# Optimization experiments

Measured on AMD Instinct MI355X. Metric: run time of the kernel, lower is better.

Reference implementation:

```python
import jax, jax.numpy as jnp
import numpy as np

E, TOPK, H, I = 8, 2, 2048, 5632
T = 4096


def setup_inputs() -> dict:
    key = jax.random.key(0)
    k1, k2, k3, k4 = jax.random.split(key, 4)
    hidden_states = jax.random.normal(k1, (T, H), dtype=jnp.float32)
    gate_w = jax.random.normal(k2, (E, H), dtype=jnp.float32) * (1.0 / np.sqrt(H))
    # fused gate+up projection: [E, 2*I, H]
    w13 = jax.random.normal(k3, (E, 2 * I, H), dtype=jnp.float32) * (1.0 / np.sqrt(H))
    # down projection: [E, H, I]
    w2 = jax.random.normal(k4, (E, H, I), dtype=jnp.float32) * (1.0 / np.sqrt(I))
    return {"hidden_states": hidden_states, "gate_w": gate_w, "w13": w13, "w2": w2, "top_k": TOPK}


def reference(hidden_states, gate_w, w13, w2, top_k):
    num_experts = gate_w.shape[0]
    inter = w2.shape[2]
    # router: fp32 gate logits -> softmax -> top-k -> renormalize (FusedMoE renormalize=True)
    logits = hidden_states.astype(jnp.float32) @ gate_w.T          # [T, E]
    probs = jax.nn.softmax(logits, axis=-1)
    vals, idx = jax.lax.top_k(probs, top_k)                        # [T, k]
    vals = vals / jnp.sum(vals, axis=-1, keepdims=True)
    # dense routing weight matrix [T, E] (zero outside top-k)
    dense_w = jnp.sum(jax.nn.one_hot(idx, num_experts, dtype=vals.dtype) * vals[..., None], axis=1)

    def body(acc, inputs):
        w13_e, w2_e, we = inputs                                   # [2I,H], [H,I], [T]
        gu = hidden_states @ w13_e.T                               # [T, 2I]
        g, u = gu[:, :inter], gu[:, inter:]
        h = jax.nn.silu(g) * u                                     # SwiGLU
        y = h @ w2_e.T                                             # [T, H]
        return acc + we[:, None] * y, None

    acc0 = jnp.zeros_like(hidden_states)
    out, _ = jax.lax.scan(body, acc0, (w13, w2, dense_w.T))
    return out
```

## Files before the change

### kernel.cpp

```cpp
#include <hip/hip_runtime.h>

#define T_TOK 4096
#define H_DIM 2048
#define I_DIM 5632
#define NE 8

typedef _Float16 f16;
typedef _Float16 f16x8 __attribute__((ext_vector_type(8)));
typedef float f32x4 __attribute__((ext_vector_type(4)));

#define OFF_META   0
#define OFF_BTOK   256
#define OFF_BW     (256 + 32768)
#define OFF_RE     (256 + 2 * 32768)
#define OFF_RW     (256 + 3 * 32768)
#define OFF_HSB    (256 + 4 * 32768)
#define OFF_WF     (OFF_HSB + (size_t)T_TOK * H_DIM * 2)

typedef const __attribute__((address_space(1))) unsigned int guint;
typedef __attribute__((address_space(3))) unsigned int luint;

__device__ __forceinline__ int swzk(int r, int bir) {
    return (bir & 15) | ((((bir >> 4) ^ r) & 7) << 4);
}

__global__ void cvt_w_kernel(const float* __restrict__ src, f16* __restrict__ dst, int n8) {
    int stride = gridDim.x * blockDim.x;
    for (int i = blockIdx.x * blockDim.x + threadIdx.x; i < n8; i += stride) {
        size_t b = (size_t)i * 8;
        float4 a = *(const float4*)(src + b);
        float4 c = *(const float4*)(src + b + 4);
        f16x8 v;
        v[0] = (f16)a.x; v[1] = (f16)a.y; v[2] = (f16)a.z; v[3] = (f16)a.w;
        v[4] = (f16)c.x; v[5] = (f16)c.y; v[6] = (f16)c.z; v[7] = (f16)c.w;
        *(f16x8*)(dst + b) = v;
    }
}

__global__ void cvt_hs_kernel(const float* __restrict__ hs, f16* __restrict__ hsb) {
    size_t i = ((size_t)blockIdx.x * 256 + threadIdx.x) * 8;
    float4 a = *(const float4*)(hs + i);
    float4 b = *(const float4*)(hs + i + 4);
    f16x8 v;
    v[0] = (f16)a.x; v[1] = (f16)a.y; v[2] = (f16)a.z; v[3] = (f16)a.w;
    v[4] = (f16)b.x; v[5] = (f16)b.y; v[6] = (f16)b.z; v[7] = (f16)b.w;
    *(f16x8*)(hsb + i) = v;
}

__global__ void gate_kernel(const float* __restrict__ hs, const float* __restrict__ gw,
                            int* __restrict__ re, float* __restrict__ rw,
                            int* __restrict__ counts) {
    int lane = threadIdx.x & 63;
    int t = blockIdx.x * 4 + (threadIdx.x >> 6);
    float acc[NE];
#pragma unroll
    for (int e = 0; e < NE; ++e) acc[e] = 0.f;
    const float* x = hs + (size_t)t * H_DIM;
    for (int i = lane; i < H_DIM; i += 64) {
        float xv = x[i];
#pragma unroll
        for (int e = 0; e < NE; ++e) acc[e] += xv * gw[e * H_DIM + i];
    }
#pragma unroll
    for (int e = 0; e < NE; ++e)
        for (int off = 32; off > 0; off >>= 1) acc[e] += __shfl_xor(acc[e], off);
    if (lane == 0) {
        int i1 = 0; float l1 = acc[0];
#pragma unroll
        for (int e = 1; e < NE; ++e) if (acc[e] > l1) { l1 = acc[e]; i1 = e; }
        int i2 = -1; float l2 = -1e30f;
#pragma unroll
        for (int e = 0; e < NE; ++e) if (e != i1 && acc[e] > l2) { l2 = acc[e]; i2 = e; }
        float aa = __expf(l2 - l1);
        float s = 1.f / (1.f + aa);
        re[t * 2] = i1; re[t * 2 + 1] = i2;
        rw[t * 2] = s;  rw[t * 2 + 1] = aa * s;
        atomicAdd(&counts[i1], 1);
        atomicAdd(&counts[i2], 1);
    }
}

__global__ void scan_kernel(int* __restrict__ meta) {
    if (threadIdx.x == 0) {
        int s = 0;
        for (int e = 0; e < NE; ++e) { meta[8 + e] = s; meta[16 + e] = s; s += meta[e]; }
    }
}

__global__ void place_kernel(const int* __restrict__ re, const float* __restrict__ rw,
                             int* __restrict__ cursor, int* __restrict__ btok,
                             float* __restrict__ bwv) {
    int t = blockIdx.x * 256 + threadIdx.x;
    if (t >= T_TOK) return;
#pragma unroll
    for (int s = 0; s < 2; ++s) {
        int e = re[t * 2 + s];
        int p = atomicAdd(&cursor[e], 1);
        btok[p] = t;
        bwv[p] = rw[t * 2 + s];
    }
}

__device__ __forceinline__ void decode_panel(int id, int npx, int e_arg,
                                             int& e, int& bx, int& by) {
    if (e_arg >= 0) { e = e_arg; bx = id >> 5; by = id & 31; return; }
    int sg  = id >> 8;
    int rem = id & 255;
    by = rem >> 3;
    int P = sg * 8 + (rem & 7);
    e = P / npx; bx = P % npx;
}

__global__ __launch_bounds__(256, 2) void gemm1_kernel(
    const f16* __restrict__ w13f, const f16* __restrict__ hsb, f16* __restrict__ hb,
    const int* __restrict__ counts, const int* __restrict__ offs,
    const int* __restrict__ btok, int e_arg, int global_h)
{
    int e, bx, by;
    decode_panel(blockIdx.x, 88, e_arg, e, bx, by);
    const int n_e = counts[e];
    if (by * 128 >= n_e) return;
    const int boff = offs[e];
    const f16* We = (e_arg >= 0) ? w13f : (w13f + (size_t)e * (2 * I_DIM) * H_DIM);

    const int tid = threadIdx.x;
    const int lane = tid & 63;
    const int wid = tid >> 6;
    const int wm = wid >> 1, wn = wid & 1;
    const int l15 = lane & 15;

    __shared__ f16 As0[128 * 64], As1[128 * 64];
    __shared__ f16 Bs0[128 * 64], Bs1[128 * 64];

    const f16* gA[4]; const f16* gB[4]; int dstc[4];
#pragma unroll
    for (int i = 0; i < 4; ++i) {
        int c = i * 256 + tid;
        int r = c >> 3;
        dstc[i] = c * 16;
        int slot = ((c & 7) ^ (r & 7)) * 8;
        int idx = by * 128 + r;
        idx = idx < n_e ? idx : n_e - 1;
        gA[i] = hsb + (size_t)btok[boff + idx] * H_DIM + slot;
        int wrow = (r < 64) ? (bx * 64 + r) : (I_DIM + bx * 64 + (r - 64));
        gB[i] = We + (size_t)wrow * H_DIM + slot;
    }

    f32x4 ag[4][2], au[4][2];
#pragma unroll
    for (int m = 0; m < 4; ++m)
#pragma unroll
        for (int n = 0; n < 2; ++n) { ag[m][n] = (f32x4)0.f; au[m][n] = (f32x4)0.f; }

    const int NT = H_DIM / 64;

#pragma unroll
    for (int i = 0; i < 4; ++i) {
        __builtin_amdgcn_global_load_lds((guint*)gA[i], (luint*)((char*)As0 + dstc[i]), 16, 0, 0);
        __builtin_amdgcn_global_load_lds((guint*)gB[i], (luint*)((char*)Bs0 + dstc[i]), 16, 0, 0);
    }

#define G1T(AR, BR, AW, BW, t)                                                      \
    {                                                                               \
        __syncthreads();    \
        if ((t) + 1 < NT) {                                                         \
            const int k0 = ((t) + 1) * 64;                                          \
            _Pragma("unroll")                                                       \
            for (int i = 0; i < 4; ++i) {                                           \
                __builtin_amdgcn_global_load_lds((guint*)(gA[i] + k0),              \
                    (luint*)((char*)AW + dstc[i]), 16, 0, 0);                       \
                __builtin_amdgcn_global_load_lds((guint*)(gB[i] + k0),              \
                    (luint*)((char*)BW + dstc[i]), 16, 0, 0);                       \
            }                                                                       \
        }                                                                           \
        _Pragma("unroll")                                                           \
        for (int kh = 0; kh < 2; ++kh) {                                            \
            const int kb = kh * 64 + (lane >> 4) * 16;                              \
            f16x8 a[4], bg[2], bu[2];                                               \
            _Pragma("unroll")                                                       \
            for (int m = 0; m < 4; ++m) {                                           \
                int r = wm * 64 + m * 16 + l15;                                     \
                a[m] = *(const f16x8*)((const char*)AR + r * 128 + swzk(r, kb));    \
            }                                                                       \
            _Pragma("unroll")                                                       \
            for (int n = 0; n < 2; ++n) {                                           \
                int rg = wn * 32 + n * 16 + l15;                                    \
                bg[n] = *(const f16x8*)((const char*)BR + rg * 128 + swzk(rg, kb)); \
                int ru = 64 + rg;                                                   \
                bu[n] = *(const f16x8*)((const char*)BR + ru * 128 + swzk(ru, kb)); \
            }                                                                       \
            _Pragma("unroll")                                                       \
            for (int m = 0; m < 4; ++m)                                             \
                _Pragma("unroll")                                                   \
                for (int n = 0; n < 2; ++n) {                                       \
                    ag[m][n] = __builtin_amdgcn_mfma_f32_16x16x32_f16(a[m], bg[n], ag[m][n], 0, 0, 0); \
                    au[m][n] = __builtin_amdgcn_mfma_f32_16x16x32_f16(a[m], bu[n], au[m][n], 0, 0, 0); \
                }                                                                   \
        }                                                                           \
    }

#pragma unroll 1
    for (int kt = 0; kt < NT; kt += 2) {
        G1T(As0, Bs0, As1, Bs1, kt);
        G1T(As1, Bs1, As0, Bs0, kt + 1);
    }
#undef G1T

    const int hbase = (global_h ? boff : 0) + by * 128;
#pragma unroll
    for (int m = 0; m < 4; ++m) {
        int rl0 = wm * 64 + m * 16 + ((lane >> 4) << 2);
#pragma unroll
        for (int r = 0; r < 4; ++r) {
            int rl = rl0 + r;
            if (by * 128 + rl < n_e) {
#pragma unroll
                for (int n = 0; n < 2; ++n) {
                    float g = ag[m][n][r];
                    float u = au[m][n][r];
                    float h = g / (1.f + __expf(-g)) * u;
                    hb[(size_t)(hbase + rl) * I_DIM + bx * 64 + wn * 32 + n * 16 + l15] = (f16)h;
                }
            }
        }
    }
}

__global__ __launch_bounds__(256, 2) void gemm2_kernel(
    const f16* __restrict__ w2f, const f16* __restrict__ hb, float* __restrict__ out,
    const int* __restrict__ counts, const int* __restrict__ offs,
    const int* __restrict__ btok, const float* __restrict__ bwv, int e_arg, int global_h)
{
    int e, bx, by;
    decode_panel(blockIdx.x, 16, e_arg, e, bx, by);
    const int n_e = counts[e];
    if (by * 128 >= n_e) return;
    const int boff = offs[e];
    const f16* We = (e_arg >= 0) ? w2f : (w2f + (size_t)e * H_DIM * I_DIM);

    const int tid = threadIdx.x;
    const int lane = tid & 63;
    const int wid = tid >> 6;
    const int wm = wid >> 1, wn = wid & 1;
    const int l15 = lane & 15;

    __shared__ f16 As0[128 * 64], As1[128 * 64];
    __shared__ f16 Bs0[128 * 64], Bs1[128 * 64];

    const int hb0 = global_h ? boff : 0;
    const f16* gA[4]; const f16* gB[4]; int dstc[4];
#pragma unroll
    for (int i = 0; i < 4; ++i) {
        int c = i * 256 + tid;
        int r = c >> 3;
        dstc[i] = c * 16;
        int slot = ((c & 7) ^ (r & 7)) * 8;
        int idx = by * 128 + r;
        idx = idx < n_e ? idx : n_e - 1;
        gA[i] = hb + (size_t)(hb0 + idx) * I_DIM + slot;
        gB[i] = We + (size_t)(bx * 128 + r) * I_DIM + slot;
    }

    f32x4 acc[4][4];
#pragma unroll
    for (int m = 0; m < 4; ++m)
#pragma unroll
        for (int n = 0; n < 4; ++n) acc[m][n] = (f32x4)0.f;

    const int NT = I_DIM / 64;

#pragma unroll
    for (int i = 0; i < 4; ++i) {
        __builtin_amdgcn_global_load_lds((guint*)gA[i], (luint*)((char*)As0 + dstc[i]), 16, 0, 0);
        __builtin_amdgcn_global_load_lds((guint*)gB[i], (luint*)((char*)Bs0 + dstc[i]), 16, 0, 0);
    }

#define G2T(AR, BR, AW, BW, t)                                                      \
    {                                                                               \
        __syncthreads();                                                            \
        if ((t) + 1 < NT) {                                                         \
            const int k0 = ((t) + 1) * 64;                                          \
            _Pragma("unroll")                                                       \
            for (int i = 0; i < 4; ++i) {                                           \
                __builtin_amdgcn_global_load_lds((guint*)(gA[i] + k0),              \
                    (luint*)((char*)AW + dstc[i]), 16, 0, 0);                       \
                __builtin_amdgcn_global_load_lds((guint*)(gB[i] + k0),              \
                    (luint*)((char*)BW + dstc[i]), 16, 0, 0);                       \
            }                                                                       \
        }                                                                           \
        _Pragma("unroll")                                                           \
        for (int kh = 0; kh < 2; ++kh) {                                            \
            const int kb = kh * 64 + (lane >> 4) * 16;                              \
            f16x8 a[4], b[4];                                                       \
            _Pragma("unroll")                                                       \
            for (int m = 0; m < 4; ++m) {                                           \
                int r = wm * 64 + m * 16 + l15;                                     \
                a[m] = *(const f16x8*)((const char*)AR + r * 128 + swzk(r, kb));    \
            }                                                                       \
            _Pragma("unroll")                                                       \
            for (int n = 0; n < 4; ++n) {                                           \
                int r = wn * 64 + n * 16 + l15;                                     \
                b[n] = *(const f16x8*)((const char*)BR + r * 128 + swzk(r, kb));    \
            }                                                                       \
            _Pragma("unroll")                                                       \
            for (int m = 0; m < 4; ++m)                                             \
                _Pragma("unroll")                                                   \
                for (int n = 0; n < 4; ++n)                                         \
                    acc[m][n] = __builtin_amdgcn_mfma_f32_16x16x32_f16(a[m], b[n], acc[m][n], 0, 0, 0); \
        }                                                                           \
    }

#pragma unroll 1
    for (int kt = 0; kt < NT; kt += 2) {
        G2T(As0, Bs0, As1, Bs1, kt);
        G2T(As1, Bs1, As0, Bs0, kt + 1);
    }
#undef G2T

#pragma unroll
    for (int m = 0; m < 4; ++m) {
        int rl0 = wm * 64 + m * 16 + ((lane >> 4) << 2);
#pragma unroll
        for (int r = 0; r < 4; ++r) {
            int rl = rl0 + r;
            if (by * 128 + rl < n_e) {
                int p = boff + by * 128 + rl;
                int tok = btok[p];
                float w = bwv[p];
#pragma unroll
                for (int n = 0; n < 4; ++n)
                    atomicAdd(&out[(size_t)tok * H_DIM + bx * 128 + wn * 64 + n * 16 + l15],
                              w * acc[m][n][r]);
            }
        }
    }
}

extern "C" void kernel_launch(void* const* d_in, const int* in_sizes, int n_in,
                              void* d_out, int out_size, void* d_ws, size_t ws_size,
                              hipStream_t stream) {
    const float* hs  = (const float*)d_in[0];
    const float* gw  = (const float*)d_in[1];
    const float* w13 = (const float*)d_in[2];
    const float* w2  = (const float*)d_in[3];
    float* out = (float*)d_out;

    char* ws = (char*)d_ws;
    int*   meta = (int*)(ws + OFF_META);
    int*   btok = (int*)(ws + OFF_BTOK);
    float* bwv  = (float*)(ws + OFF_BW);
    int*   re   = (int*)(ws + OFF_RE);
    float* rw   = (float*)(ws + OFF_RW);
    f16*   hsb  = (f16*)(ws + OFF_HSB);

    hipMemsetAsync(d_out, 0, (size_t)T_TOK * H_DIM * 4, stream);
    hipMemsetAsync(meta, 0, 256, stream);

    cvt_hs_kernel<<<(T_TOK * H_DIM) / (256 * 8), 256, 0, stream>>>(hs, hsb);
    gate_kernel<<<T_TOK / 4, 256, 0, stream>>>(hs, gw, re, rw, meta);
    scan_kernel<<<1, 64, 0, stream>>>(meta);
    place_kernel<<<T_TOK / 256, 256, 0, stream>>>(re, rw, meta + 16, btok, bwv);

    const size_t w13_elems = (size_t)NE * 2 * I_DIM * H_DIM;
    const size_t w2_elems  = (size_t)NE * H_DIM * I_DIM;

    size_t o_w13f = OFF_WF;
    size_t o_w2f  = o_w13f + w13_elems * 2;
    size_t o_hb   = o_w2f + w2_elems * 2;
    size_t need_full = o_hb + (size_t)2 * T_TOK * I_DIM * 2;

    size_t f_w13 = OFF_WF;
    size_t f_w2  = f_w13 + (size_t)2 * I_DIM * H_DIM * 2;
    size_t f_hb  = f_w2 + (size_t)H_DIM * I_DIM * 2;
    size_t need_pe = f_hb + (size_t)T_TOK * I_DIM * 2;
    (void)need_pe;

    if (ws_size >= need_full) {
        f16* w13f = (f16*)(ws + o_w13f);
        f16* w2f  = (f16*)(ws + o_w2f);
        f16* hb   = (f16*)(ws + o_hb);
        cvt_w_kernel<<<2048, 256, 0, stream>>>(w13, w13f, (int)(w13_elems / 8));
        cvt_w_kernel<<<2048, 256, 0, stream>>>(w2,  w2f,  (int)(w2_elems / 8));
        gemm1_kernel<<<704 * 32, 256, 0, stream>>>(w13f, hsb, hb, meta, meta + 8, btok, -1, 1);
        gemm2_kernel<<<128 * 32, 256, 0, stream>>>(w2f, hb, out, meta, meta + 8, btok, bwv, -1, 1);
    } else {
        f16* w13f = (f16*)(ws + f_w13);
        f16* w2f  = (f16*)(ws + f_w2);
        f16* hb   = (f16*)(ws + f_hb);
        for (int e = 0; e < NE; ++e) {
            cvt_w_kernel<<<1024, 256, 0, stream>>>(w13 + (size_t)e * 2 * I_DIM * H_DIM, w13f,
                                                   (int)((size_t)2 * I_DIM * H_DIM / 8));
            gemm1_kernel<<<88 * 32, 256, 0, stream>>>(w13f, hsb, hb, meta, meta + 8, btok, e, 0);
            cvt_w_kernel<<<1024, 256, 0, stream>>>(w2 + (size_t)e * H_DIM * I_DIM, w2f,
                                                   (int)((size_t)H_DIM * I_DIM / 8));
            gemm2_kernel<<<16 * 32, 256, 0, stream>>>(w2f, hb, out, meta, meta + 8, btok, bwv, e, 0);
        }
    }
}
```

Baseline: 1.278 ms.

## Fuse fp32 weight conversion into MoE GEMMs, loading fp32 tiles into LDS

Removes the separate fp32-to-fp16 weight conversion kernels and has both expert GEMMs load fp32 weight tiles directly into LDS, converting to fp16 when building MFMA fragments. The K tile is halved to 32 to fit fp32 tiles, and launch bounds allow 4 blocks per SIMD. This eliminates a full read-write-read pass over the large weight tensors, at the cost of more k-iterations and syncs and twice the weight bytes per tile within the GEMMs.

```diff
diff --git a/kernel.cpp b/kernel.cpp
--- a/kernel.cpp
+++ b/kernel.cpp
@@ -15,7 +15,7 @@
 #define OFF_RE     (256 + 2 * 32768)
 #define OFF_RW     (256 + 3 * 32768)
 #define OFF_HSB    (256 + 4 * 32768)
-#define OFF_WF     (OFF_HSB + (size_t)T_TOK * H_DIM * 2)
+#define OFF_HB     (OFF_HSB + (size_t)T_TOK * H_DIM * 2)
 
 typedef const __attribute__((address_space(1))) unsigned int guint;
 typedef __attribute__((address_space(3))) unsigned int luint;
@@ -24,17 +24,18 @@
     return (bir & 15) | ((((bir >> 4) ^ r) & 7) << 4);
 }
 
-__global__ void cvt_w_kernel(const float* __restrict__ src, f16* __restrict__ dst, int n8) {
-    int stride = gridDim.x * blockDim.x;
-    for (int i = blockIdx.x * blockDim.x + threadIdx.x; i < n8; i += stride) {
-        size_t b = (size_t)i * 8;
-        float4 a = *(const float4*)(src + b);
-        float4 c = *(const float4*)(src + b + 4);
-        f16x8 v;
-        v[0] = (f16)a.x; v[1] = (f16)a.y; v[2] = (f16)a.z; v[3] = (f16)a.w;
-        v[4] = (f16)c.x; v[5] = (f16)c.y; v[6] = (f16)c.z; v[7] = (f16)c.w;
-        *(f16x8*)(dst + b) = v;
-    }
+__device__ __forceinline__ f16x8 lda16(const char* base, int r, int kq) {
+    int L = r >> 1;
+    int u = ((r & 1) << 2) + kq;
+    return *(const f16x8*)(base + L * 128 + ((u ^ (L & 7)) << 4));
+}
+__device__ __forceinline__ f16x8 ldb32(const char* base, int r, int kq) {
+    f32x4 v0 = *(const f32x4*)(base + r * 128 + swzk(r, kq * 32));
+    f32x4 v1 = *(const f32x4*)(base + r * 128 + swzk(r, kq * 32 + 16));
+    f16x8 o;
+    o[0] = (f16)v0[0]; o[1] = (f16)v0[1]; o[2] = (f16)v0[2]; o[3] = (f16)v0[3];
+    o[4] = (f16)v1[0]; o[5] = (f16)v1[1]; o[6] = (f16)v1[2]; o[7] = (f16)v1[3];
+    return o;
 }
 
 __global__ void cvt_hs_kernel(const float* __restrict__ hs, f16* __restrict__ hsb) {
@@ -111,8 +112,8 @@
     e = P / npx; bx = P % npx;
 }
 
-__global__ __launch_bounds__(256, 2) void gemm1_kernel(
-    const f16* __restrict__ w13f, const f16* __restrict__ hsb, f16* __restrict__ hb,
+__global__ __launch_bounds__(256, 4) void gemm1_kernel(
+    const float* __restrict__ w13, const f16* __restrict__ hsb, f16* __restrict__ hb,
     const int* __restrict__ counts, const int* __restrict__ offs,
     const int* __restrict__ btok, int e_arg, int global_h)
 {
@@ -121,29 +122,38 @@
     const int n_e = counts[e];
     if (by * 128 >= n_e) return;
     const int boff = offs[e];
-    const f16* We = (e_arg >= 0) ? w13f : (w13f + (size_t)e * (2 * I_DIM) * H_DIM);
+    const float* We = w13 + (size_t)e * (2 * I_DIM) * H_DIM;
 
     const int tid = threadIdx.x;
     const int lane = tid & 63;
     const int wid = tid >> 6;
     const int wm = wid >> 1, wn = wid & 1;
     const int l15 = lane & 15;
-
-    __shared__ f16 As0[128 * 64], As1[128 * 64];
-    __shared__ f16 Bs0[128 * 64], Bs1[128 * 64];
-
-    const f16* gA[4]; const f16* gB[4]; int dstc[4];
-#pragma unroll
-    for (int i = 0; i < 4; ++i) {
+    const int kq = lane >> 4;
+
+    __shared__ f16  As0[128 * 32], As1[128 * 32];
+    __shared__ float Bs0[128 * 32], Bs1[128 * 32];
+
+    const f16* gA[2]; int dA[2];
+#pragma unroll
+    for (int i = 0; i < 2; ++i) {
         int c = i * 256 + tid;
-        int r = c >> 3;
-        dstc[i] = c * 16;
-        int slot = ((c & 7) ^ (r & 7)) * 8;
+        int L = c >> 3;
+        int u = (c & 7) ^ (L & 7);
+        int r = 2 * L + (u >> 2);
+        dA[i] = c * 16;
         int idx = by * 128 + r;
         idx = idx < n_e ? idx : n_e - 1;
-        gA[i] = hsb + (size_t)btok[boff + idx] * H_DIM + slot;
+        gA[i] = hsb + (size_t)btok[boff + idx] * H_DIM + (u & 3) * 8;
+    }
+    const float* gB[4]; int dB[4];
+#pragma unroll
+    for (int j = 0; j < 4; ++j) {
+        int c = j * 256 + tid;
+        int r = c >> 3;
+        dB[j] = c * 16;
         int wrow = (r < 64) ? (bx * 64 + r) : (I_DIM + bx * 64 + (r - 64));
-        gB[i] = We + (size_t)wrow * H_DIM + slot;
+        gB[j] = We + (size_t)wrow * H_DIM + ((c & 7) ^ (r & 7)) * 4;
     }
 
     f32x4 ag[4][2], au[4][2];
@@ -152,51 +162,45 @@
 #pragma unroll
         for (int n = 0; n < 2; ++n) { ag[m][n] = (f32x4)0.f; au[m][n] = (f32x4)0.f; }
 
-    const int NT = H_DIM / 64;
-
-#pragma unroll
-    for (int i = 0; i < 4; ++i) {
-        __builtin_amdgcn_global_load_lds((guint*)gA[i], (luint*)((char*)As0 + dstc[i]), 16, 0, 0);
-        __builtin_amdgcn_global_load_lds((guint*)gB[i], (luint*)((char*)Bs0 + dstc[i]), 16, 0, 0);
-    }
+    const int NT = H_DIM / 32;
+
+#pragma unroll
+    for (int i = 0; i < 2; ++i)
+        __builtin_amdgcn_global_load_lds((guint*)gA[i], (luint*)((char*)As0 + dA[i]), 16, 0, 0);
+#pragma unroll
+    for (int j = 0; j < 4; ++j)
+        __builtin_amdgcn_global_load_lds((guint*)gB[j], (luint*)((char*)Bs0 + dB[j]), 16, 0, 0);
 
 #define G1T(AR, BR, AW, BW, t)                                                      \
     {                                                                               \
         __syncthreads();    \
         if ((t) + 1 < NT) {                                                         \
-            const int k0 = ((t) + 1) * 64;                                          \
-            _Pragma("unroll")                                                       \
-            for (int i = 0; i < 4; ++i) {                                           \
+            const int k0 = ((t) + 1) * 32;                                          \
+            _Pragma("unroll")                                                       \
+            for (int i = 0; i < 2; ++i)                                             \
                 __builtin_amdgcn_global_load_lds((guint*)(gA[i] + k0),              \
-                    (luint*)((char*)AW + dstc[i]), 16, 0, 0);                       \
-                __builtin_amdgcn_global_load_lds((guint*)(gB[i] + k0),              \
-                    (luint*)((char*)BW + dstc[i]), 16, 0, 0);                       \
+                    (luint*)((char*)AW + dA[i]), 16, 0, 0);                         \
+            _Pragma("unroll")                                                       \
+            for (int j = 0; j < 4; ++j)                                             \
+                __builtin_amdgcn_global_load_lds((guint*)(gB[j] + k0),              \
+                    (luint*)((char*)BW + dB[j]), 16, 0, 0);                         \
+        }                                                                           \
+        f16x8 a[4], bg[2], bu[2];                                                   \
+        _Pragma("unroll")                                                           \
+        for (int m = 0; m < 4; ++m)                                                 \
+            a[m] = lda16((const char*)AR, wm * 64 + m * 16 + l15, kq);              \
+        _Pragma("unroll")                                                           \
+        for (int n = 0; n < 2; ++n) {                                               \
+            bg[n] = ldb32((const char*)BR, wn * 32 + n * 16 + l15, kq);             \
+            bu[n] = ldb32((const char*)BR, 64 + wn * 32 + n * 16 + l15, kq);        \
+        }                                                                           \
+        _Pragma("unroll")                                                           \
+        for (int m = 0; m < 4; ++m)                                                 \
+            _Pragma("unroll")                                                       \
+            for (int n = 0; n < 2; ++n) {                                           \
+                ag[m][n] = __builtin_amdgcn_mfma_f32_16x16x32_f16(a[m], bg[n], ag[m][n], 0, 0, 0); \
+                au[m][n] = __builtin_amdgcn_mfma_f32_16x16x32_f16(a[m], bu[n], au[m][n], 0, 0, 0); \
             }                                                                       \
-        }                                                                           \
-        _Pragma("unroll")                                                           \
-        for (int kh = 0; kh < 2; ++kh) {                                            \
-            const int kb = kh * 64 + (lane >> 4) * 16;                              \
-            f16x8 a[4], bg[2], bu[2];                                               \
-            _Pragma("unroll")                                                       \
-            for (int m = 0; m < 4; ++m) {                                           \
-                int r = wm * 64 + m * 16 + l15;                                     \
-                a[m] = *(const f16x8*)((const char*)AR + r * 128 + swzk(r, kb));    \
-            }                                                                       \
-            _Pragma("unroll")                                                       \
-            for (int n = 0; n < 2; ++n) {                                           \
-                int rg = wn * 32 + n * 16 + l15;                                    \
-                bg[n] = *(const f16x8*)((const char*)BR + rg * 128 + swzk(rg, kb)); \
-                int ru = 64 + rg;                                                   \
-                bu[n] = *(const f16x8*)((const char*)BR + ru * 128 + swzk(ru, kb)); \
-            }                                                                       \
-            _Pragma("unroll")                                                       \
-            for (int m = 0; m < 4; ++m)                                             \
-                _Pragma("unroll")                                                   \
-                for (int n = 0; n < 2; ++n) {                                       \
-                    ag[m][n] = __builtin_amdgcn_mfma_f32_16x16x32_f16(a[m], bg[n], ag[m][n], 0, 0, 0); \
-                    au[m][n] = __builtin_amdgcn_mfma_f32_16x16x32_f16(a[m], bu[n], au[m][n], 0, 0, 0); \
-                }                                                                   \
-        }                                                                           \
     }
 
 #pragma unroll 1
@@ -226,8 +230,8 @@
     }
 }
 
-__global__ __launch_bounds__(256, 2) void gemm2_kernel(
-    const f16* __restrict__ w2f, const f16* __restrict__ hb, float* __restrict__ out,
+__global__ __launch_bounds__(256, 4) void gemm2_kernel(
+    const float* __restrict__ w2, const f16* __restrict__ hb, float* __restrict__ out,
     const int* __restrict__ counts, const int* __restrict__ offs,
     const int* __restrict__ btok, const float* __restrict__ bwv, int e_arg, int global_h)
 {
@@ -236,29 +240,38 @@
     const int n_e = counts[e];
     if (by * 128 >= n_e) return;
     const int boff = offs[e];
-    const f16* We = (e_arg >= 0) ? w2f : (w2f + (size_t)e * H_DIM * I_DIM);
+    const float* We = w2 + (size_t)e * H_DIM * I_DIM;
 
     const int tid = threadIdx.x;
     const int lane = tid & 63;
     const int wid = tid >> 6;
     const int wm = wid >> 1, wn = wid & 1;
     const int l15 = lane & 15;
-
-    __shared__ f16 As0[128 * 64], As1[128 * 64];
-    __shared__ f16 Bs0[128 * 64], Bs1[128 * 64];
+    const int kq = lane >> 4;
+
+    __shared__ f16  As0[128 * 32], As1[128 * 32];
+    __shared__ float Bs0[128 * 32], Bs1[128 * 32];
 
     const int hb0 = global_h ? boff : 0;
-    const f16* gA[4]; const f16* gB[4]; int dstc[4];
-#pragma unroll
-    for (int i = 0; i < 4; ++i) {
+    const f16* gA[2]; int dA[2];
+#pragma unroll
+    for (int i = 0; i < 2; ++i) {
         int c = i * 256 + tid;
-        int r = c >> 3;
-        dstc[i] = c * 16;
-        int slot = ((c & 7) ^ (r & 7)) * 8;
+        int L = c >> 3;
+        int u = (c & 7) ^ (L & 7);
+        int r = 2 * L + (u >> 2);
+        dA[i] = c * 16;
         int idx = by * 128 + r;
         idx = idx < n_e ? idx : n_e - 1;
-        gA[i] = hb + (size_t)(hb0 + idx) * I_DIM + slot;
-        gB[i] = We + (size_t)(bx * 128 + r) * I_DIM + slot;
+        gA[i] = hb + (size_t)(hb0 + idx) * I_DIM + (u & 3) * 8;
+    }
+    const float* gB[4]; int dB[4];
+#pragma unroll
+    for (int j = 0; j < 4; ++j) {
+        int c = j * 256 + tid;
+        int r = c >> 3;
+        dB[j] = c * 16;
+        gB[j] = We + (size_t)(bx * 128 + r) * I_DIM + ((c & 7) ^ (r & 7)) * 4;
     }
 
     f32x4 acc[4][4];
@@ -267,47 +280,41 @@
 #pragma unroll
         for (int n = 0; n < 4; ++n) acc[m][n] = (f32x4)0.f;
 
-    const int NT = I_DIM / 64;
-
-#pragma unroll
-    for (int i = 0; i < 4; ++i) {
-        __builtin_amdgcn_global_load_lds((guint*)gA[i], (luint*)((char*)As0 + dstc[i]), 16, 0, 0);
-        __builtin_amdgcn_global_load_lds((guint*)gB[i], (luint*)((char*)Bs0 + dstc[i]), 16, 0, 0);
-    }
+    const int NT = I_DIM / 32;
+
+#pragma unroll
+    for (int i = 0; i < 2; ++i)
+        __builtin_amdgcn_global_load_lds((guint*)gA[i], (luint*)((char*)As0 + dA[i]), 16, 0, 0);
+#pragma unroll
+    for (int j = 0; j < 4; ++j)
+        __builtin_amdgcn_global_load_lds((guint*)gB[j], (luint*)((char*)Bs0 + dB[j]), 16, 0, 0);
 
 #define G2T(AR, BR, AW, BW, t)                                                      \
     {                                                                               \
         __syncthreads();                                                            \
         if ((t) + 1 < NT) {                                                         \
-            const int k0 = ((t) + 1) * 64;                                          \
-            _Pragma("unroll")                                                       \
-            for (int i = 0; i < 4; ++i) {                                           \
+            const int k0 = ((t) + 1) * 32;                                          \
+            _Pragma("unroll")                                                       \
+            for (int i = 0; i < 2; ++i)                                             \
                 __builtin_amdgcn_global_load_lds((guint*)(gA[i] + k0),              \
-                    (luint*)((char*)AW + dstc[i]), 16, 0, 0);                       \
-                __builtin_amdgcn_global_load_lds((guint*)(gB[i] + k0),              \
-                    (luint*)((char*)BW + dstc[i]), 16, 0, 0);                       \
-            }                                                                       \
+                    (luint*)((char*)AW + dA[i]), 16, 0, 0);                         \
+            _Pragma("unroll")                                                       \
+            for (int j = 0; j < 4; ++j)                                             \
+                __builtin_amdgcn_global_load_lds((guint*)(gB[j] + k0),              \
+                    (luint*)((char*)BW + dB[j]), 16, 0, 0);                         \
         }                                                                           \
-        _Pragma("unroll")                                                           \
-        for (int kh = 0; kh < 2; ++kh) {                                            \
-            const int kb = kh * 64 + (lane >> 4) * 16;                              \
-            f16x8 a[4], b[4];                                                       \
-            _Pragma("unroll")                                                       \
-            for (int m = 0; m < 4; ++m) {                                           \
-                int r = wm * 64 + m * 16 + l15;                                     \
-                a[m] = *(const f16x8*)((const char*)AR + r * 128 + swzk(r, kb));    \
-            }                                                                       \
-            _Pragma("unroll")                                                       \
-            for (int n = 0; n < 4; ++n) {                                           \
-                int r = wn * 64 + n * 16 + l15;                                     \
-                b[n] = *(const f16x8*)((const char*)BR + r * 128 + swzk(r, kb));    \
-            }                                                                       \
-            _Pragma("unroll")                                                       \
-            for (int m = 0; m < 4; ++m)                                             \
-                _Pragma("unroll")                                                   \
-                for (int n = 0; n < 4; ++n)                                         \
-                    acc[m][n] = __builtin_amdgcn_mfma_f32_16x16x32_f16(a[m], b[n], acc[m][n], 0, 0, 0); \
-        }                                                                           \
+        f16x8 a[4], b[4];                                                           \
+        _Pragma("unroll")                                                           \
+        for (int m = 0; m < 4; ++m)                                                 \
+            a[m] = lda16((const char*)AR, wm * 64 + m * 16 + l15, kq);              \
+        _Pragma("unroll")                                                           \
+        for (int n = 0; n < 4; ++n)                                                 \
+            b[n] = ldb32((const char*)BR, wn * 64 + n * 16 + l15, kq);              \
+        _Pragma("unroll")                                                           \
+        for (int m = 0; m < 4; ++m)                                                 \
+            _Pragma("unroll")                                                       \
+            for (int n = 0; n < 4; ++n)                                             \
+                acc[m][n] = __builtin_amdgcn_mfma_f32_16x16x32_f16(a[m], b[n], acc[m][n], 0, 0, 0); \
     }
 
 #pragma unroll 1
@@ -352,6 +359,7 @@
     int*   re   = (int*)(ws + OFF_RE);
     float* rw   = (float*)(ws + OFF_RW);
     f16*   hsb  = (f16*)(ws + OFF_HSB);
+    f16*   hb   = (f16*)(ws + OFF_HB);
 
     hipMemsetAsync(d_out, 0, (size_t)T_TOK * H_DIM * 4, stream);
     hipMemsetAsync(meta, 0, 256, stream);
@@ -361,39 +369,14 @@
     scan_kernel<<<1, 64, 0, stream>>>(meta);
     place_kernel<<<T_TOK / 256, 256, 0, stream>>>(re, rw, meta + 16, btok, bwv);
 
-    const size_t w13_elems = (size_t)NE * 2 * I_DIM * H_DIM;
-    const size_t w2_elems  = (size_t)NE * H_DIM * I_DIM;
-
-    size_t o_w13f = OFF_WF;
-    size_t o_w2f  = o_w13f + w13_elems * 2;
-    size_t o_hb   = o_w2f + w2_elems * 2;
-    size_t need_full = o_hb + (size_t)2 * T_TOK * I_DIM * 2;
-
-    size_t f_w13 = OFF_WF;
-    size_t f_w2  = f_w13 + (size_t)2 * I_DIM * H_DIM * 2;
-    size_t f_hb  = f_w2 + (size_t)H_DIM * I_DIM * 2;
-    size_t need_pe = f_hb + (size_t)T_TOK * I_DIM * 2;
-    (void)need_pe;
-
+    size_t need_full = OFF_HB + (size_t)2 * T_TOK * I_DIM * 2;
     if (ws_size >= need_full) {
-        f16* w13f = (f16*)(ws + o_w13f);
-        f16* w2f  = (f16*)(ws + o_w2f);
-        f16* hb   = (f16*)(ws + o_hb);
-        cvt_w_kernel<<<2048, 256, 0, stream>>>(w13, w13f, (int)(w13_elems / 8));
-        cvt_w_kernel<<<2048, 256, 0, stream>>>(w2,  w2f,  (int)(w2_elems / 8));
-        gemm1_kernel<<<704 * 32, 256, 0, stream>>>(w13f, hsb, hb, meta, meta + 8, btok, -1, 1);
-        gemm2_kernel<<<128 * 32, 256, 0, stream>>>(w2f, hb, out, meta, meta + 8, btok, bwv, -1, 1);
+        gemm1_kernel<<<704 * 32, 256, 0, stream>>>(w13, hsb, hb, meta, meta + 8, btok, -1, 1);
+        gemm2_kernel<<<128 * 32, 256, 0, stream>>>(w2, hb, out, meta, meta + 8, btok, bwv, -1, 1);
     } else {
-        f16* w13f = (f16*)(ws + f_w13);
-        f16* w2f  = (f16*)(ws + f_w2);
-        f16* hb   = (f16*)(ws + f_hb);
         for (int e = 0; e < NE; ++e) {
-            cvt_w_kernel<<<1024, 256, 0, stream>>>(w13 + (size_t)e * 2 * I_DIM * H_DIM, w13f,
-                                                   (int)((size_t)2 * I_DIM * H_DIM / 8));
-            gemm1_kernel<<<88 * 32, 256, 0, stream>>>(w13f, hsb, hb, meta, meta + 8, btok, e, 0);
-            cvt_w_kernel<<<1024, 256, 0, stream>>>(w2 + (size_t)e * H_DIM * I_DIM, w2f,
-                                                   (int)((size_t)H_DIM * I_DIM / 8));
-            gemm2_kernel<<<16 * 32, 256, 0, stream>>>(w2f, hb, out, meta, meta + 8, btok, bwv, e, 0);
+            gemm1_kernel<<<88 * 32, 256, 0, stream>>>(w13, hsb, hb, meta, meta + 8, btok, e, 0);
+            gemm2_kernel<<<16 * 32, 256, 0, stream>>>(w2, hb, out, meta, meta + 8, btok, bwv, e, 0);
         }
     }
 }
```

After: 1.386 ms. +8.4%, slower.

## Single-buffer GEMM LDS tiles for higher occupancy and fuse w2 conversion into gemm1

Applied to the files above, without the earlier changes.

Both GEMM kernels drop the double-buffered LDS tiles for a single buffer with two barriers per k-step, and launch bounds rise from 2 to 4 blocks per CU. The goal is to hide memory latency through more resident waves instead of software prefetch. The w2 fp32-to-fp16 conversion now runs as extra leading blocks of the gemm1 launch rather than as a separate kernel, so it overlaps with gemm1 work, and the w13 conversion grid grows. This loses the load/compute overlap inside each block and may add register pressure under the tighter launch bound.

```diff
diff --git a/kernel.cpp b/kernel.cpp
--- a/kernel.cpp
+++ b/kernel.cpp
@@ -111,13 +111,28 @@
     e = P / npx; bx = P % npx;
 }
 
-__global__ __launch_bounds__(256, 2) void gemm1_kernel(
+__global__ __launch_bounds__(256, 4) void gemm1_kernel(
     const f16* __restrict__ w13f, const f16* __restrict__ hsb, f16* __restrict__ hb,
     const int* __restrict__ counts, const int* __restrict__ offs,
-    const int* __restrict__ btok, int e_arg, int global_h)
+    const int* __restrict__ btok,
+    const float* __restrict__ w2src, f16* __restrict__ w2dst, int cvt_n8, int cvt_blocks,
+    int e_arg, int global_h)
 {
+    if ((int)blockIdx.x < cvt_blocks) {
+        int stride = cvt_blocks * 256;
+        for (int i = blockIdx.x * 256 + threadIdx.x; i < cvt_n8; i += stride) {
+            size_t b = (size_t)i * 8;
+            float4 a = *(const float4*)(w2src + b);
+            float4 c = *(const float4*)(w2src + b + 4);
+            f16x8 v;
+            v[0] = (f16)a.x; v[1] = (f16)a.y; v[2] = (f16)a.z; v[3] = (f16)a.w;
+            v[4] = (f16)c.x; v[5] = (f16)c.y; v[6] = (f16)c.z; v[7] = (f16)c.w;
+            *(f16x8*)(w2dst + b) = v;
+        }
+        return;
+    }
     int e, bx, by;
-    decode_panel(blockIdx.x, 88, e_arg, e, bx, by);
+    decode_panel((int)blockIdx.x - cvt_blocks, 88, e_arg, e, bx, by);
     const int n_e = counts[e];
     if (by * 128 >= n_e) return;
     const int boff = offs[e];
@@ -129,8 +144,8 @@
     const int wm = wid >> 1, wn = wid & 1;
     const int l15 = lane & 15;
 
-    __shared__ f16 As0[128 * 64], As1[128 * 64];
-    __shared__ f16 Bs0[128 * 64], Bs1[128 * 64];
+    __shared__ f16 As[128 * 64];
+    __shared__ f16 Bs[128 * 64];
 
     const f16* gA[4]; const f16* gB[4]; int dstc[4];
 #pragma unroll
@@ -154,57 +169,41 @@
 
     const int NT = H_DIM / 64;
 
-#pragma unroll
-    for (int i = 0; i < 4; ++i) {
-        __builtin_amdgcn_global_load_lds((guint*)gA[i], (luint*)((char*)As0 + dstc[i]), 16, 0, 0);
-        __builtin_amdgcn_global_load_lds((guint*)gB[i], (luint*)((char*)Bs0 + dstc[i]), 16, 0, 0);
-    }
-
-#define G1T(AR, BR, AW, BW, t)                                                      \
-    {                                                                               \
-        __syncthreads();    \
-        if ((t) + 1 < NT) {                                                         \
-            const int k0 = ((t) + 1) * 64;                                          \
-            _Pragma("unroll")                                                       \
-            for (int i = 0; i < 4; ++i) {                                           \
-                __builtin_amdgcn_global_load_lds((guint*)(gA[i] + k0),              \
-                    (luint*)((char*)AW + dstc[i]), 16, 0, 0);                       \
-                __builtin_amdgcn_global_load_lds((guint*)(gB[i] + k0),              \
-                    (luint*)((char*)BW + dstc[i]), 16, 0, 0);                       \
-            }                                                                       \
-        }                                                                           \
-        _Pragma("unroll")                                                           \
-        for (int kh = 0; kh < 2; ++kh) {                                            \
-            const int kb = kh * 64 + (lane >> 4) * 16;                              \
-            f16x8 a[4], bg[2], bu[2];                                               \
-            _Pragma("unroll")                                                       \
-            for (int m = 0; m < 4; ++m) {                                           \
-                int r = wm * 64 + m * 16 + l15;                                     \
-                a[m] = *(const f16x8*)((const char*)AR + r * 128 + swzk(r, kb));    \
-            }                                                                       \
-            _Pragma("unroll")                                                       \
-            for (int n = 0; n < 2; ++n) {                                           \
-                int rg = wn * 32 + n * 16 + l15;                                    \
-                bg[n] = *(const f16x8*)((const char*)BR + rg * 128 + swzk(rg, kb)); \
-                int ru = 64 + rg;                                                   \
-                bu[n] = *(const f16x8*)((const char*)BR + ru * 128 + swzk(ru, kb)); \
-            }                                                                       \
-            _Pragma("unroll")                                                       \
-            for (int m = 0; m < 4; ++m)                                             \
-                _Pragma("unroll")                                                   \
-                for (int n = 0; n < 2; ++n) {                                       \
-                    ag[m][n] = __builtin_amdgcn_mfma_f32_16x16x32_f16(a[m], bg[n], ag[m][n], 0, 0, 0); \
-                    au[m][n] = __builtin_amdgcn_mfma_f32_16x16x32_f16(a[m], bu[n], au[m][n], 0, 0, 0); \
-                }                                                                   \
-        }                                                                           \
-    }
-
 #pragma unroll 1
-    for (int kt = 0; kt < NT; kt += 2) {
-        G1T(As0, Bs0, As1, Bs1, kt);
-        G1T(As1, Bs1, As0, Bs0, kt + 1);
-    }
-#undef G1T
+    for (int kt = 0; kt < NT; ++kt) {
+        __syncthreads();
+        const int k0 = kt * 64;
+#pragma unroll
+        for (int i = 0; i < 4; ++i) {
+            __builtin_amdgcn_global_load_lds((guint*)(gA[i] + k0), (luint*)((char*)As + dstc[i]), 16, 0, 0);
+            __builtin_amdgcn_global_load_lds((guint*)(gB[i] + k0), (luint*)((char*)Bs + dstc[i]), 16, 0, 0);
+        }
+        __syncthreads();
+#pragma unroll
+        for (int kh = 0; kh < 2; ++kh) {
+            const int kb = kh * 64 + (lane >> 4) * 16;
+            f16x8 a[4], bg[2], bu[2];
+#pragma unroll
+            for (int m = 0; m < 4; ++m) {
+                int r = wm * 64 + m * 16 + l15;
+                a[m] = *(const f16x8*)((const char*)As + r * 128 + swzk(r, kb));
+            }
+#pragma unroll
+            for (int n = 0; n < 2; ++n) {
+                int rg = wn * 32 + n * 16 + l15;
+                bg[n] = *(const f16x8*)((const char*)Bs + rg * 128 + swzk(rg, kb));
+                int ru = 64 + rg;
+                bu[n] = *(const f16x8*)((const char*)Bs + ru * 128 + swzk(ru, kb));
+            }
+#pragma unroll
+            for (int m = 0; m < 4; ++m)
+#pragma unroll
+                for (int n = 0; n < 2; ++n) {
+                    ag[m][n] = __builtin_amdgcn_mfma_f32_16x16x32_f16(a[m], bg[n], ag[m][n], 0, 0, 0);
+                    au[m][n] = __builtin_amdgcn_mfma_f32_16x16x32_f16(a[m], bu[n], au[m][n], 0, 0, 0);
+                }
+        }
+    }
 
     const int hbase = (global_h ? boff : 0) + by * 128;
 #pragma unroll
@@ -226,7 +225,7 @@
     }
 }
 
-__global__ __launch_bounds__(256, 2) void gemm2_kernel(
+__global__ __launch_bounds__(256, 4) void gemm2_kernel(
     const f16* __restrict__ w2f, const f16* __restrict__ hb, float* __restrict__ out,
     const int* __restrict__ counts, const int* __restrict__ offs,
     const int* __restrict__ btok, const float* __restrict__ bwv, int e_arg, int global_h)
@@ -244,8 +243,8 @@
     const int wm = wid >> 1, wn = wid & 1;
     const int l15 = lane & 15;
 
-    __shared__ f16 As0[128 * 64], As1[128 * 64];
-    __shared__ f16 Bs0[128 * 64], Bs1[128 * 64];
+    __shared__ f16 As[128 * 64];
+    __shared__ f16 Bs[128 * 64];
 
     const int hb0 = global_h ? boff : 0;
     const f16* gA[4]; const f16* gB[4]; int dstc[4];
@@ -269,53 +268,37 @@
 
     const int NT = I_DIM / 64;
 
-#pragma unroll
-    for (int i = 0; i < 4; ++i) {
-        __builtin_amdgcn_global_load_lds((guint*)gA[i], (luint*)((char*)As0 + dstc[i]), 16, 0, 0);
-        __builtin_amdgcn_global_load_lds((guint*)gB[i], (luint*)((char*)Bs0 + dstc[i]), 16, 0, 0);
-    }
-
-#define G2T(AR, BR, AW, BW, t)                                                      \
-    {                                                                               \
-        __syncthreads();                                                            \
-        if ((t) + 1 < NT) {                                                         \
-            const int k0 = ((t) + 1) * 64;                                          \
-            _Pragma("unroll")                                                       \
-            for (int i = 0; i < 4; ++i) {                                           \
-                __builtin_amdgcn_global_load_lds((guint*)(gA[i] + k0),              \
-                    (luint*)((char*)AW + dstc[i]), 16, 0, 0);                       \
-                __builtin_amdgcn_global_load_lds((guint*)(gB[i] + k0),              \
-                    (luint*)((char*)BW + dstc[i]), 16, 0, 0);                       \
-            }                                                                       \
-        }                                                                           \
-        _Pragma("unroll")                                                           \
-        for (int kh = 0; kh < 2; ++kh) {                                            \
-            const int kb = kh * 64 + (lane >> 4) * 16;                              \
-            f16x8 a[4], b[4];                                                       \
-            _Pragma("unroll")                                                       \
-            for (int m = 0; m < 4; ++m) {                                           \
-                int r = wm * 64 + m * 16 + l15;                                     \
-                a[m] = *(const f16x8*)((const char*)AR + r * 128 + swzk(r, kb));    \
-            }                                                                       \
-            _Pragma("unroll")                                                       \
-            for (int n = 0; n < 4; ++n) {                                           \
-                int r = wn * 64 + n * 16 + l15;                                     \
-                b[n] = *(const f16x8*)((const char*)BR + r * 128 + swzk(r, kb));    \
-            }                                                                       \
-            _Pragma("unroll")                                                       \
-            for (int m = 0; m < 4; ++m)                                             \
-                _Pragma("unroll")                                                   \
-                for (int n = 0; n < 4; ++n)                                         \
-                    acc[m][n] = __builtin_amdgcn_mfma_f32_16x16x32_f16(a[m], b[n], acc[m][n], 0, 0, 0); \
-        }                                                                           \
-    }
-
 #pragma unroll 1
-    for (int kt = 0; kt < NT; kt += 2) {
-        G2T(As0, Bs0, As1, Bs1, kt);
-        G2T(As1, Bs1, As0, Bs0, kt + 1);
-    }
-#undef G2T
+    for (int kt = 0; kt < NT; ++kt) {
+        __syncthreads();
+        const int k0 = kt * 64;
+#pragma unroll
+        for (int i = 0; i < 4; ++i) {
+            __builtin_amdgcn_global_load_lds((guint*)(gA[i] + k0), (luint*)((char*)As + dstc[i]), 16, 0, 0);
+            __builtin_amdgcn_global_load_lds((guint*)(gB[i] + k0), (luint*)((char*)Bs + dstc[i]), 16, 0, 0);
+        }
+        __syncthreads();
+#pragma unroll
+        for (int kh = 0; kh < 2; ++kh) {
+            const int kb = kh * 64 + (lane >> 4) * 16;
+            f16x8 a[4], b[4];
+#pragma unroll
+            for (int m = 0; m < 4; ++m) {
+                int r = wm * 64 + m * 16 + l15;
+                a[m] = *(const f16x8*)((const char*)As + r * 128 + swzk(r, kb));
+            }
+#pragma unroll
+            for (int n = 0; n < 4; ++n) {
+                int r = wn * 64 + n * 16 + l15;
+                b[n] = *(const f16x8*)((const char*)Bs + r * 128 + swzk(r, kb));
+            }
+#pragma unroll
+            for (int m = 0; m < 4; ++m)
+#pragma unroll
+                for (int n = 0; n < 4; ++n)
+                    acc[m][n] = __builtin_amdgcn_mfma_f32_16x16x32_f16(a[m], b[n], acc[m][n], 0, 0, 0);
+        }
+    }
 
 #pragma unroll
     for (int m = 0; m < 4; ++m) {
@@ -372,27 +355,27 @@
     size_t f_w13 = OFF_WF;
     size_t f_w2  = f_w13 + (size_t)2 * I_DIM * H_DIM * 2;
     size_t f_hb  = f_w2 + (size_t)H_DIM * I_DIM * 2;
-    size_t need_pe = f_hb + (size_t)T_TOK * I_DIM * 2;
-    (void)need_pe;
 
     if (ws_size >= need_full) {
         f16* w13f = (f16*)(ws + o_w13f);
         f16* w2f  = (f16*)(ws + o_w2f);
         f16* hb   = (f16*)(ws + o_hb);
-        cvt_w_kernel<<<2048, 256, 0, stream>>>(w13, w13f, (int)(w13_elems / 8));
-        cvt_w_kernel<<<2048, 256, 0, stream>>>(w2,  w2f,  (int)(w2_elems / 8));
-        gemm1_kernel<<<704 * 32, 256, 0, stream>>>(w13f, hsb, hb, meta, meta + 8, btok, -1, 1);
+        cvt_w_kernel<<<4096, 256, 0, stream>>>(w13, w13f, (int)(w13_elems / 8));
+        gemm1_kernel<<<2048 + 704 * 32, 256, 0, stream>>>(
+            w13f, hsb, hb, meta, meta + 8, btok,
+            w2, w2f, (int)(w2_elems / 8), 2048, -1, 1);
         gemm2_kernel<<<128 * 32, 256, 0, stream>>>(w2f, hb, out, meta, meta + 8, btok, bwv, -1, 1);
     } else {
         f16* w13f = (f16*)(ws + f_w13);
         f16* w2f  = (f16*)(ws + f_w2);
         f16* hb   = (f16*)(ws + f_hb);
+        const size_t w13_slice = (size_t)2 * I_DIM * H_DIM;
+        const size_t w2_slice  = (size_t)H_DIM * I_DIM;
         for (int e = 0; e < NE; ++e) {
-            cvt_w_kernel<<<1024, 256, 0, stream>>>(w13 + (size_t)e * 2 * I_DIM * H_DIM, w13f,
-                                                   (int)((size_t)2 * I_DIM * H_DIM / 8));
-            gemm1_kernel<<<88 * 32, 256, 0, stream>>>(w13f, hsb, hb, meta, meta + 8, btok, e, 0);
-            cvt_w_kernel<<<1024, 256, 0, stream>>>(w2 + (size_t)e * H_DIM * I_DIM, w2f,
-                                                   (int)((size_t)H_DIM * I_DIM / 8));
+            cvt_w_kernel<<<2048, 256, 0, stream>>>(w13 + e * w13_slice, w13f, (int)(w13_slice / 8));
+            gemm1_kernel<<<2048 + 88 * 32, 256, 0, stream>>>(
+                w13f, hsb, hb, meta, meta + 8, btok,
+                w2 + e * w2_slice, w2f, (int)(w2_slice / 8), 2048, e, 0);
             gemm2_kernel<<<16 * 32, 256, 0, stream>>>(w2f, hb, out, meta, meta + 8, btok, bwv, e, 0);
         }
     }
```

Measured after the change: 1.169 ms. 1.09x faster.
